# Kernel optimization log

Hardware: AMD Instinct MI355X
Metric: run time of the kernel (lower is better)

The kernel has to match this reference:

```python
import jax, jax.numpy as jnp
import numpy as np

B, S, H, R, IN, OPS, NPAD = 128, 128, 512, 16, 2, 5, 16
L = IN + NPAD
NEG = -1e12


def setup_inputs():
    key = jax.random.key(0)
    ks = jax.random.split(key, 32)
    def n(k, shape, scale=1.0):
        return jax.random.normal(k, shape, jnp.float32) * scale
    s = 0.05
    return {
        "encoder_outputs": n(ks[0], (S, B, H)),
        "current_emb": n(ks[1], (B, 1, H)),
        "left_childs": n(ks[2], (B, H)),
        "padding_hidden": jnp.zeros((1, H), jnp.float32),
        "num_pades": n(ks[3], (B, NPAD, H)),
        "rule_scores": n(ks[4], (R, H)),
        "embedding_weight": n(ks[5], (1, IN, H)),
        "W_concat_l": n(ks[6], (H, H), s), "b_concat_l": jnp.zeros((H,)),
        "W_concat_lg": n(ks[7], (H, H), s), "b_concat_lg": jnp.zeros((H,)),
        "W_concat_r": n(ks[8], (2 * H, H), s), "b_concat_r": jnp.zeros((H,)),
        "W_concat_rg": n(ks[9], (2 * H, H), s), "b_concat_rg": jnp.zeros((H,)),
        "W_tree_attn": n(ks[10], (2 * H, H), s), "b_tree_attn": jnp.zeros((H,)),
        "W_tree_score": n(ks[11], (H, 1), s), "b_tree_score": jnp.zeros((1,)),
        "W_rule_attn": n(ks[12], (2 * H, H), s), "b_rule_attn": jnp.zeros((H,)),
        "W_rule_score": n(ks[13], (H, 1), s), "b_rule_score": jnp.zeros((1,)),
        "W_rp1": n(ks[14], (H, H), s), "b_rp1": jnp.zeros((H,)),
        "W_rp2": n(ks[15], (H, 1), s), "b_rp2": jnp.zeros((1,)),
        "W_sc_attn": n(ks[16], (3 * H, H), s), "b_sc_attn": jnp.zeros((H,)),
        "W_sc_score": n(ks[17], (H, 1), s),
        "W_ops": n(ks[18], (2 * H, OPS), s), "b_ops": jnp.zeros((OPS,)),
        "seq_mask": jax.random.randint(ks[19], (B, S), 0, 2).astype(jnp.int32),
        "mask_nums": jax.random.randint(ks[20], (B, L), 0, 2).astype(jnp.int32),
        "has_left": jax.random.randint(ks[21], (B,), 0, 2).astype(jnp.int32),
        "stack_empty": jax.random.randint(ks[22], (B,), 0, 2).astype(jnp.int32),
    }


def reference(encoder_outputs, current_emb, left_childs, padding_hidden, num_pades,
              rule_scores, embedding_weight,
              W_concat_l, b_concat_l, W_concat_lg, b_concat_lg,
              W_concat_r, b_concat_r, W_concat_rg, b_concat_rg,
              W_tree_attn, b_tree_attn, W_tree_score, b_tree_score,
              W_rule_attn, b_rule_attn, W_rule_score, b_rule_score,
              W_rp1, b_rp1, W_rp2, b_rp2,
              W_sc_attn, b_sc_attn, W_sc_score, W_ops, b_ops,
              seq_mask, mask_nums, has_left, stack_empty):
    sm = seq_mask.astype(bool)          # [B,S] True = pad
    nm = mask_nums.astype(bool)         # [B,L]
    hl = has_left.astype(bool)[:, None]
    se = stack_empty.astype(bool)[:, None]
    h = encoder_outputs.shape[-1]
    # gather top-of-stack embedding, padding for empty stacks (the ragged python loop)
    c = jnp.where(se, padding_hidden[0], current_emb[:, 0])  # [B,H]
    # gated combine: left_child==None branch vs cat(left, c) branch (dropout=eval)
    node_l = jnp.tanh(c @ W_concat_l + b_concat_l) * jax.nn.sigmoid(c @ W_concat_lg + b_concat_lg)
    node_r = (jnp.tanh(left_childs @ W_concat_r[:h] + c @ W_concat_r[h:] + b_concat_r)
              * jax.nn.sigmoid(left_childs @ W_concat_rg[:h] + c @ W_concat_rg[h:] + b_concat_rg))
    q = jnp.where(hl, node_r, node_l)                        # [B,H]
    current_node = q[:, None, :]                              # [B,1,H]
    # TreeAttn: concat(hidden, enc) -> Linear -> tanh -> Linear(H,1) -> softmax over S
    e = jnp.tanh(q @ W_tree_attn[:h] + encoder_outputs @ W_tree_attn[h:] + b_tree_attn)  # [S,B,H]
    ae = (e @ W_tree_score)[..., 0] + b_tree_score[0]         # [S,B]
    ae = jnp.where(sm, NEG, ae.T)                             # [B,S]
    current_attn = jax.nn.softmax(ae, axis=1)                 # [B,S]
    current_context = jnp.einsum('bs,sbh->bh', current_attn, encoder_outputs)[:, None, :]
    # RuleAttn: concat(enc, rule) additive attention, softmax over S
    re = jnp.tanh(encoder_outputs @ W_rule_attn[:h]
                  + (rule_scores @ W_rule_attn[h:])[:, None, None, :]
                  + b_rule_attn)                              # [R,S,B,H]
    r_ae = (re @ W_rule_score)[..., 0] + b_rule_score[0]      # [R,S,B]
    r_ae = jnp.transpose(r_ae, (2, 0, 1))                     # [B,R,S]
    r_ae = jnp.where(sm[:, None, :], NEG, r_ae)
    rules_attn = jax.nn.softmax(r_ae, axis=-1)
    rules_context = jnp.einsum('brs,sbh->brh', rules_attn + 0.2 * current_attn[:, None, :], encoder_outputs)
    rule_prob = jax.nn.softmax((jnp.tanh(rules_context @ W_rp1 + b_rp1) @ W_rp2)[..., 0] + b_rp2[0], axis=-1)  # [B,R]
    # leaf scoring: Score(cat(node, context), [const_embs | num_pades])
    bsz = q.shape[0]
    ew = jnp.concatenate([jnp.broadcast_to(embedding_weight, (bsz,) + embedding_weight.shape[1:]), num_pades], axis=1)  # [B,L,H]
    leaf = jnp.concatenate([q, current_context[:, 0]], axis=1)  # [B,2H]
    sc = jnp.tanh((leaf @ W_sc_attn[:2 * h])[:, None, :] + ew @ W_sc_attn[2 * h:] + b_sc_attn)  # [B,L,H]
    num_score = jnp.where(nm, NEG, (sc @ W_sc_score)[..., 0])   # [B,L]
    op = leaf @ W_ops + b_ops                                   # [B,OPS]
    return num_score, op, current_node, current_context, ew, rule_prob
```

## Files before the change

kernel.cpp:

```cpp
#include <hip/hip_runtime.h>
#include <hip/hip_bf16.h>

#define B_ 128
#define S_ 128
#define H_ 512
#define R_ 16
#define IN_ 2
#define OPS_ 5
#define NPAD_ 16
#define L_ 18
#define NEGV (-1000000000000.0f)
#define C2_ (-2.885390081777927f)

typedef __bf16 bf16_t;
typedef bf16_t bf16x8 __attribute__((ext_vector_type(8)));
typedef float floatx4 __attribute__((ext_vector_type(4)));

__device__ __forceinline__ float rcp_f(float x) { return __builtin_amdgcn_rcpf(x); }
__device__ __forceinline__ float exp2_f(float x) { return __builtin_amdgcn_exp2f(x); }

__device__ __forceinline__ float fast_tanh(float x) {
    return 2.0f * rcp_f(1.0f + exp2_f(C2_ * x)) - 1.0f;
}
__device__ __forceinline__ float fast_sigmoid(float x) {
    return rcp_f(1.0f + exp2_f(-1.4426950408889634f * x));
}
__device__ __forceinline__ unsigned short f2bf(float f) {
    unsigned int u = __builtin_bit_cast(unsigned int, f);
    u += 0x7fff + ((u >> 16) & 1);
    return (unsigned short)(u >> 16);
}
__device__ __forceinline__ float bf2f(unsigned short u) {
    return __builtin_bit_cast(float, (unsigned int)u << 16);
}

__device__ __forceinline__ void glds16(const void* g, void* l) {
    __builtin_amdgcn_global_load_lds(
        (const __attribute__((address_space(1))) void*)g,
        (__attribute__((address_space(3))) void*)l, 16, 0, 0);
}

#define LROW 32
#define LBUF 4096

__device__ __forceinline__ void mfma_tile(const unsigned short* __restrict__ A,
                                          const unsigned short* __restrict__ Bt,
                                          void* __restrict__ Cv, bool bf16_out,
                                          int m0, int n0, int K, int ldc,
                                          unsigned short* As, unsigned short* Bs) {
    const int tid  = threadIdx.x;
    const int w    = tid >> 6, lane = tid & 63;
    const int quad = lane >> 4, mn = lane & 15;
    const int wm = (w & 1) * 64, wn = (w >> 1) * 64;
    const int sr = tid >> 2;
    const int csw = ((tid & 3) ^ ((tid >> 3) & 3)) * 8;
    const int qs  = (quad ^ ((mn >> 1) & 3)) * 8;

    const unsigned short* pa0 = A  + (size_t)(m0 + sr)      * K + csw;
    const unsigned short* pa1 = A  + (size_t)(m0 + sr + 64) * K + csw;
    const unsigned short* pb0 = Bt + (size_t)(n0 + sr)      * K + csw;
    const unsigned short* pb1 = Bt + (size_t)(n0 + sr + 64) * K + csw;

    const int wbase = w * 512;
    glds16(pa0, As + wbase);
    glds16(pa1, As + wbase + 2048);
    glds16(pb0, Bs + wbase);
    glds16(pb1, Bs + wbase + 2048);
    __syncthreads();

    floatx4 acc[4][4] = {};

    for (int k0 = 0; k0 < K; k0 += 32) {
        const int cur = (k0 >> 5) & 1;
        const unsigned short* Asb = As + cur * LBUF;
        const unsigned short* Bsb = Bs + cur * LBUF;

        if (k0 + 32 < K) {
            const int nb = cur ^ 1;
            glds16(pa0 + k0 + 32, As + nb * LBUF + wbase);
            glds16(pa1 + k0 + 32, As + nb * LBUF + wbase + 2048);
            glds16(pb0 + k0 + 32, Bs + nb * LBUF + wbase);
            glds16(pb1 + k0 + 32, Bs + nb * LBUF + wbase + 2048);
        }

        bf16x8 af[4], bfr[4];
        #pragma unroll
        for (int i = 0; i < 4; ++i)
            af[i] = *(const bf16x8*)&Asb[(wm + i * 16 + mn) * LROW + qs];
        #pragma unroll
        for (int j = 0; j < 4; ++j)
            bfr[j] = *(const bf16x8*)&Bsb[(wn + j * 16 + mn) * LROW + qs];

        #pragma unroll
        for (int i = 0; i < 4; ++i)
            #pragma unroll
            for (int j = 0; j < 4; ++j)
                acc[i][j] = __builtin_amdgcn_mfma_f32_16x16x32_bf16(bfr[j], af[i], acc[i][j], 0, 0, 0);

        __syncthreads();
    }

    #pragma unroll
    for (int i = 0; i < 4; ++i) {
        int row = m0 + wm + i * 16 + mn;
        #pragma unroll
        for (int j = 0; j < 4; ++j) {
            int col = n0 + wn + j * 16 + quad * 4;
            if (bf16_out) {
                ushort4 v = {f2bf(acc[i][j][0]), f2bf(acc[i][j][1]),
                             f2bf(acc[i][j][2]), f2bf(acc[i][j][3])};
                *(ushort4*)((unsigned short*)Cv + (size_t)row * ldc + col) = v;
            } else {
                float4 v = {acc[i][j][0], acc[i][j][1], acc[i][j][2], acc[i][j][3]};
                *(float4*)((float*)Cv + (size_t)row * ldc + col) = v;
            }
        }
    }
}

__global__ __launch_bounds__(256) void k_gemm_mega1(const unsigned short* __restrict__ EO_bf,
                                                    const unsigned short* __restrict__ Wcat,
                                                    unsigned short* __restrict__ eobuf,
                                                    const unsigned short* __restrict__ q_bf,
                                                    const unsigned short* __restrict__ T5,
                                                    float* __restrict__ qT) {
    __shared__ unsigned short As[2 * LBUF];
    __shared__ unsigned short Bs[2 * LBUF];
    int blk = blockIdx.x;
    if (blk < 1024)
        mfma_tile(EO_bf, Wcat, eobuf, true, (blk & 127) * 128, (blk >> 7) * 128, 512, 1024, As, Bs);
    else
        mfma_tile(q_bf, T5, qT, false, 0, (blk - 1024) * 128, 512, 512, As, Bs);
}

__global__ __launch_bounds__(256) void k_gemm_mega2(const unsigned short* __restrict__ rctx_bf,
                                                    const unsigned short* __restrict__ T8,
                                                    float* __restrict__ rclin,
                                                    const unsigned short* __restrict__ leaf_bf,
                                                    const unsigned short* __restrict__ T9,
                                                    float* __restrict__ lsb,
                                                    const unsigned short* __restrict__ ew_bf,
                                                    const unsigned short* __restrict__ T10,
                                                    unsigned short* __restrict__ ewp_bf) {
    __shared__ unsigned short As[2 * LBUF];
    __shared__ unsigned short Bs[2 * LBUF];
    int blk = blockIdx.x;
    if (blk < 64)
        mfma_tile(rctx_bf, T8, rclin, false, (blk >> 2) * 128, (blk & 3) * 128, 512, 512, As, Bs);
    else if (blk < 68)
        mfma_tile(leaf_bf, T9, lsb, false, 0, (blk - 64) * 128, 1024, 512, As, Bs);
    else {
        int r = blk - 68;
        mfma_tile(ew_bf, T10, ewp_bf, true, (r >> 2) * 128, (r & 3) * 128, 512, 512, As, Bs);
    }
}

struct MJ5 {
    const unsigned short* A[5]; const unsigned short* Bt[5]; float* C[5];
    int M[5]; int K[5];
};
__global__ __launch_bounds__(256) void gemm_bf16_j5(MJ5 g) {
    __shared__ unsigned short As[2 * LBUF];
    __shared__ unsigned short Bs[2 * LBUF];

    const int z = blockIdx.z;
    const unsigned short* A  = g.A[z];
    const unsigned short* Bt = g.Bt[z];
    float* C = g.C[z];
    const int M = g.M[z], K = g.K[z];

    const int tid  = threadIdx.x;
    const int w    = tid >> 6, lane = tid & 63;
    const int quad = lane >> 4, mn = lane & 15;
    const int wm = (w & 1) * 64, wn = (w >> 1) * 64;
    const int n0 = blockIdx.x * 128;

    const int sr = tid >> 2;
    const int csw = ((tid & 3) ^ ((tid >> 3) & 3)) * 8;
    const int qs  = (quad ^ ((mn >> 1) & 3)) * 8;
    const int ra0 = min(sr, M - 1);
    const int ra1 = min(sr + 64, M - 1);

    const unsigned short* pa0 = A  + (size_t)ra0 * K + csw;
    const unsigned short* pa1 = A  + (size_t)ra1 * K + csw;
    const unsigned short* pb0 = Bt + (size_t)(n0 + sr)      * K + csw;
    const unsigned short* pb1 = Bt + (size_t)(n0 + sr + 64) * K + csw;

    const int wbase = w * 512;
    glds16(pa0, As + wbase);
    glds16(pa1, As + wbase + 2048);
    glds16(pb0, Bs + wbase);
    glds16(pb1, Bs + wbase + 2048);
    __syncthreads();

    floatx4 acc[4][4] = {};

    for (int k0 = 0; k0 < K; k0 += 32) {
        const int cur = (k0 >> 5) & 1;
        const unsigned short* Asb = As + cur * LBUF;
        const unsigned short* Bsb = Bs + cur * LBUF;

        if (k0 + 32 < K) {
            const int nb = cur ^ 1;
            glds16(pa0 + k0 + 32, As + nb * LBUF + wbase);
            glds16(pa1 + k0 + 32, As + nb * LBUF + wbase + 2048);
            glds16(pb0 + k0 + 32, Bs + nb * LBUF + wbase);
            glds16(pb1 + k0 + 32, Bs + nb * LBUF + wbase + 2048);
        }

        bf16x8 af[4], bfr[4];
        #pragma unroll
        for (int i = 0; i < 4; ++i)
            af[i] = *(const bf16x8*)&Asb[(wm + i * 16 + mn) * LROW + qs];
        #pragma unroll
        for (int j = 0; j < 4; ++j)
            bfr[j] = *(const bf16x8*)&Bsb[(wn + j * 16 + mn) * LROW + qs];

        #pragma unroll
        for (int i = 0; i < 4; ++i)
            #pragma unroll
            for (int j = 0; j < 4; ++j)
                acc[i][j] = __builtin_amdgcn_mfma_f32_16x16x32_bf16(bfr[j], af[i], acc[i][j], 0, 0, 0);

        __syncthreads();
    }

    #pragma unroll
    for (int i = 0; i < 4; ++i) {
        int row = wm + i * 16 + mn;
        if (row < M) {
            #pragma unroll
            for (int j = 0; j < 4; ++j) {
                int col = n0 + wn + j * 16 + quad * 4;
                float4 v = {acc[i][j][0], acc[i][j][1], acc[i][j][2], acc[i][j][3]};
                *(float4*)(C + (size_t)row * 512 + col) = v;
            }
        }
    }
}

struct PrepArgs {
    const float *EO, *cur, *padh, *left, *rsc, *embw, *npad;
    const int* se;
    unsigned short *EO_bf, *c_bf, *acat_bf, *rsc_bf, *ew_bf;
    float* ew_out;
    const float* tsrc[11];
    unsigned short* tdst[11];
    int tK[11];
    int tbase[12];
};
#define PG_CAST 8192
#define PG_EW   1152
#define PG_PREP 288
#define PG_WT   3584
#define PG_TOTAL (PG_CAST + PG_EW + PG_PREP + PG_WT)

__global__ __launch_bounds__(256) void k_prep_mega(PrepArgs a) {
    __shared__ float t[32][33];
    int blk = blockIdx.x, tid = threadIdx.x;
    if (blk < PG_CAST) {
        int i = (blk * 256 + tid) * 4;
        float4 v = *(const float4*)(a.EO + i);
        ushort4 o;
        o.x = f2bf(v.x); o.y = f2bf(v.y); o.z = f2bf(v.z); o.w = f2bf(v.w);
        *(ushort4*)(a.EO_bf + i) = o;
    } else if (blk < PG_CAST + PG_EW) {
        int i = ((blk - PG_CAST) * 256 + tid) * 4;
        int j = i & 511;
        int bl = i >> 9;
        int l = bl % L_;
        int b = bl / L_;
        const float* src = (l < IN_) ? (a.embw + l * H_ + j)
                                     : (a.npad + ((size_t)b * NPAD_ + (l - IN_)) * H_ + j);
        float4 v = *(const float4*)src;
        *(float4*)(a.ew_out + i) = v;
        ushort4 o;
        o.x = f2bf(v.x); o.y = f2bf(v.y); o.z = f2bf(v.z); o.w = f2bf(v.w);
        *(ushort4*)(a.ew_bf + i) = o;
    } else if (blk < PG_CAST + PG_EW + PG_PREP) {
        int i = (blk - PG_CAST - PG_EW) * 256 + tid;
        if (i < B_ * H_) {
            int b = i >> 9, j = i & 511;
            float cv = a.se[b] ? a.padh[j] : a.cur[i];
            a.c_bf[i] = f2bf(cv);
            a.acat_bf[b * 1024 + j] = f2bf(a.left[i]);
            a.acat_bf[b * 1024 + 512 + j] = f2bf(cv);
        } else {
            int k = i - B_ * H_;
            a.rsc_bf[k] = f2bf(a.rsc[k]);
        }
    } else {
        int rel = blk - (PG_CAST + PG_EW + PG_PREP);
        int j = 0;
        while (rel >= a.tbase[j + 1]) ++j;
        int r = rel - a.tbase[j];
        int K = a.tK[j];
        const float* src = a.tsrc[j];
        unsigned short* dst = a.tdst[j];
        int bx = (r & 15) * 32;
        int by = (r >> 4) * 32;
        int tx = tid & 31, ty = tid >> 5;
        #pragma unroll
        for (int i = 0; i < 32; i += 8)
            t[ty + i][tx] = src[(size_t)(by + ty + i) * 512 + bx + tx];
        __syncthreads();
        #pragma unroll
        for (int i = 0; i < 32; i += 8)
            dst[(size_t)(bx + ty + i) * K + by + tx] = f2bf(t[tx][ty + i]);
    }
}

__global__ void k_node(const float* __restrict__ gl, const float* __restrict__ glg,
                       const float* __restrict__ gr, const float* __restrict__ grg,
                       const float* __restrict__ bl, const float* __restrict__ blg,
                       const float* __restrict__ br, const float* __restrict__ brg,
                       const int* __restrict__ hl,
                       unsigned short* __restrict__ q_bf, float* __restrict__ node_out,
                       unsigned short* __restrict__ leaf_bf) {
    int i = blockIdx.x * blockDim.x + threadIdx.x;
    int b = i >> 9, j = i & 511;
    float nl = fast_tanh(gl[i] + bl[j]) * fast_sigmoid(glg[i] + blg[j]);
    float nr = fast_tanh(gr[i] + br[j]) * fast_sigmoid(grg[i] + brg[j]);
    float v = hl[b] ? nr : nl;
    node_out[i] = v;
    q_bf[i] = f2bf(v);
    leaf_bf[b * 1024 + j] = f2bf(v);
}

__global__ __launch_bounds__(256) void k_score_fused(const float* __restrict__ qT,
                                                     const unsigned short* __restrict__ eobuf,
                                                     const float* __restrict__ b_ta,
                                                     const float* __restrict__ w_ts,
                                                     const float* __restrict__ b_ts,
                                                     const float* __restrict__ RP,
                                                     const float* __restrict__ b_ra,
                                                     const float* __restrict__ w_rs,
                                                     const float* __restrict__ b_rs,
                                                     const int* __restrict__ sm,
                                                     float* __restrict__ attn,
                                                     float* __restrict__ comb) {
    __shared__ float sc[S_];
    int blk = blockIdx.x;
    int tid = threadIdx.x;
    int wid = tid >> 6, lane = tid & 63;
    int j0 = lane * 8;

    if (blk < 128) {
        int b = blk;
        float4 q0 = *(const float4*)(qT + b * H_ + j0);
        float4 q1 = *(const float4*)(qT + b * H_ + j0 + 4);
        float4 t0 = *(const float4*)(b_ta + j0);
        float4 t1 = *(const float4*)(b_ta + j0 + 4);
        float4 w0 = *(const float4*)(w_ts + j0);
        float4 w1 = *(const float4*)(w_ts + j0 + 4);
        float qc[8] = {C2_*(q0.x+t0.x), C2_*(q0.y+t0.y), C2_*(q0.z+t0.z), C2_*(q0.w+t0.w),
                       C2_*(q1.x+t1.x), C2_*(q1.y+t1.y), C2_*(q1.z+t1.z), C2_*(q1.w+t1.w)};
        float w2[8] = {2*w0.x, 2*w0.y, 2*w0.z, 2*w0.w, 2*w1.x, 2*w1.y, 2*w1.z, 2*w1.w};
        float wsum = 0.5f * (w2[0]+w2[1]+w2[2]+w2[3]+w2[4]+w2[5]+w2[6]+w2[7]);
        float bias = b_ts[0];

        for (int s = wid; s < S_; s += 4) {
            if (sm[b * S_ + s]) {
                if (lane == 0) sc[s] = NEGV;
                continue;
            }
            uint4 ev = *(const uint4*)(eobuf + ((size_t)s * B_ + b) * 1024 + j0);
            const unsigned short* ep = (const unsigned short*)&ev;
            float acc = -wsum;
            #pragma unroll
            for (int k = 0; k < 8; ++k) {
                float y = fmaf(C2_, bf2f(ep[k]), qc[k]);
                acc = fmaf(w2[k], rcp_f(1.0f + exp2_f(y)), acc);
            }
            #pragma unroll
            for (int o = 32; o > 0; o >>= 1) acc += __shfl_xor(acc, o);
            if (lane == 0) sc[s] = acc + bias;
        }
        __syncthreads();
        if (tid < 64) {
            float v0 = sc[tid], v1 = sc[tid + 64];
            float m = fmaxf(v0, v1);
            #pragma unroll
            for (int o = 32; o > 0; o >>= 1) m = fmaxf(m, __shfl_xor(m, o));
            float e0 = __expf(v0 - m), e1 = __expf(v1 - m);
            float ss = e0 + e1;
            #pragma unroll
            for (int o = 32; o > 0; o >>= 1) ss += __shfl_xor(ss, o);
            float r = rcp_f(ss);
            attn[b * S_ + tid] = e0 * r;
            attn[b * S_ + tid + 64] = e1 * r;
        }
        return;
    }

    int row = (blk - 128) * 4 + wid;
    int s = row >> 7, b = row & 127;
    bool masked = sm[b * S_ + s] != 0;
    if (masked) {
        if (lane < R_) comb[((size_t)b * R_ + lane) * S_ + s] = NEGV;
        return;
    }
    uint4 ev = *(const uint4*)(eobuf + (size_t)row * 1024 + 512 + j0);
    const unsigned short* ep = (const unsigned short*)&ev;
    float4 a0 = *(const float4*)(b_ra + j0);
    float4 a1 = *(const float4*)(b_ra + j0 + 4);
    float4 w0 = *(const float4*)(w_rs + j0);
    float4 w1 = *(const float4*)(w_rs + j0 + 4);
    float ba[8] = {a0.x, a0.y, a0.z, a0.w, a1.x, a1.y, a1.z, a1.w};
    float w2[8], ed[8];
    float wsum = 0.f;
    {
        float w[8] = {w0.x, w0.y, w0.z, w0.w, w1.x, w1.y, w1.z, w1.w};
        #pragma unroll
        for (int k = 0; k < 8; ++k) {
            wsum += w[k];
            w2[k] = 2.0f * w[k];
            ed[k] = C2_ * (bf2f(ep[k]) + ba[k]);
        }
    }
    float bias = b_rs[0];
    #pragma unroll
    for (int r = 0; r < R_; ++r) {
        float4 r0 = *(const float4*)(RP + r * H_ + j0);
        float4 r1 = *(const float4*)(RP + r * H_ + j0 + 4);
        float rp[8] = {r0.x, r0.y, r0.z, r0.w, r1.x, r1.y, r1.z, r1.w};
        float acc = -wsum;
        #pragma unroll
        for (int k = 0; k < 8; ++k) {
            float y = fmaf(C2_, rp[k], ed[k]);
            acc = fmaf(w2[k], rcp_f(1.0f + exp2_f(y)), acc);
        }
        #pragma unroll
        for (int o = 32; o > 0; o >>= 1) acc += __shfl_xor(acc, o);
        if (lane == 0) comb[((size_t)b * R_ + r) * S_ + s] = acc + bias;
    }
}

__global__ __launch_bounds__(256) void k_ctxsm(const unsigned short* __restrict__ EO_bf,
                                               const float* __restrict__ attn,
                                               const float* __restrict__ comb,
                                               const int* __restrict__ sm,
                                               float* __restrict__ ctx_out,
                                               unsigned short* __restrict__ leaf_bf,
                                               unsigned short* __restrict__ rctx) {
    __shared__ float cb2[S_ * 20];
    __shared__ float at[S_];
    __shared__ short usl[S_];
    __shared__ int ucount;
    int b = blockIdx.x;
    int tid = threadIdx.x;
    int w = tid >> 6, lane = tid & 63;

    if (tid < S_) at[tid] = attn[b * S_ + tid];
    if (tid == 0) {
        int c = 0;
        for (int s = 0; s < S_; ++s)
            if (!sm[b * S_ + s]) usl[c++] = (short)s;
        ucount = c;
    }
    __syncthreads();

    #pragma unroll
    for (int rr = 0; rr < 4; ++rr) {
        int r = w * 4 + rr;
        const float* rowp = comb + (size_t)b * R_ * S_ + r * S_;
        float v0 = rowp[lane], v1 = rowp[lane + 64];
        float m = fmaxf(v0, v1);
        #pragma unroll
        for (int o = 32; o > 0; o >>= 1) m = fmaxf(m, __shfl_xor(m, o));
        float e0 = __expf(v0 - m), e1 = __expf(v1 - m);
        float ss = e0 + e1;
        #pragma unroll
        for (int o = 32; o > 0; o >>= 1) ss += __shfl_xor(ss, o);
        float rc_ = rcp_f(ss);
        cb2[lane * 20 + r]        = e0 * rc_ + 0.2f * at[lane];
        cb2[(lane + 64) * 20 + r] = e1 * rc_ + 0.2f * at[lane + 64];
    }
    __syncthreads();

    int j = blockIdx.y * 256 + tid;
    int nu = ucount;
    float ctx = 0.f;
    float rc[R_] = {};
    for (int ii = 0; ii < nu; ++ii) {
        int s = usl[ii];
        float eo = bf2f(EO_bf[((size_t)s * B_ + b) * H_ + j]);
        float4 c0 = *(const float4*)&cb2[s * 20];
        float4 c1 = *(const float4*)&cb2[s * 20 + 4];
        float4 c2 = *(const float4*)&cb2[s * 20 + 8];
        float4 c3 = *(const float4*)&cb2[s * 20 + 12];
        ctx = fmaf(at[s], eo, ctx);
        rc[0]  = fmaf(c0.x, eo, rc[0]);  rc[1]  = fmaf(c0.y, eo, rc[1]);
        rc[2]  = fmaf(c0.z, eo, rc[2]);  rc[3]  = fmaf(c0.w, eo, rc[3]);
        rc[4]  = fmaf(c1.x, eo, rc[4]);  rc[5]  = fmaf(c1.y, eo, rc[5]);
        rc[6]  = fmaf(c1.z, eo, rc[6]);  rc[7]  = fmaf(c1.w, eo, rc[7]);
        rc[8]  = fmaf(c2.x, eo, rc[8]);  rc[9]  = fmaf(c2.y, eo, rc[9]);
        rc[10] = fmaf(c2.z, eo, rc[10]); rc[11] = fmaf(c2.w, eo, rc[11]);
        rc[12] = fmaf(c3.x, eo, rc[12]); rc[13] = fmaf(c3.y, eo, rc[13]);
        rc[14] = fmaf(c3.z, eo, rc[14]); rc[15] = fmaf(c3.w, eo, rc[15]);
    }
    ctx_out[b * H_ + j] = ctx;
    leaf_bf[b * 1024 + 512 + j] = f2bf(ctx);
    #pragma unroll
    for (int r = 0; r < R_; ++r) rctx[((size_t)b * R_ + r) * H_ + j] = f2bf(rc[r]);
}

__global__ __launch_bounds__(256) void k_epilogue(const float* __restrict__ rclin,
                                                  const float* __restrict__ b_rp1,
                                                  const float* __restrict__ w_rp2,
                                                  const float* __restrict__ b_rp2,
                                                  float* __restrict__ prob,
                                                  const float* __restrict__ lsb,
                                                  const unsigned short* __restrict__ ewp,
                                                  const float* __restrict__ b_sc,
                                                  const float* __restrict__ w_scs,
                                                  const int* __restrict__ mask_nums,
                                                  float* __restrict__ ns_out,
                                                  const unsigned short* __restrict__ leaf_bf,
                                                  const float* __restrict__ Wops,
                                                  const float* __restrict__ bops,
                                                  float* __restrict__ op_out) {
    __shared__ float sc[R_];
    int blk = blockIdx.x;
    int wid = threadIdx.x >> 6, lane = threadIdx.x & 63;
    if (blk < 128) {
        int b = blk;
        int j0 = lane * 8;
        float4 p0 = *(const float4*)(b_rp1 + j0);
        float4 p1 = *(const float4*)(b_rp1 + j0 + 4);
        float4 w0 = *(const float4*)(w_rp2 + j0);
        float4 w1 = *(const float4*)(w_rp2 + j0 + 4);
        float brc[8] = {C2_*p0.x, C2_*p0.y, C2_*p0.z, C2_*p0.w,
                        C2_*p1.x, C2_*p1.y, C2_*p1.z, C2_*p1.w};
        float w[8] = {w0.x, w0.y, w0.z, w0.w, w1.x, w1.y, w1.z, w1.w};
        float wsum = 0.f;
        #pragma unroll
        for (int k = 0; k < 8; ++k) wsum += w[k];
        #pragma unroll
        for (int rr = 0; rr < 4; ++rr) {
            int r = wid * 4 + rr;
            const float* rl = rclin + ((size_t)b * R_ + r) * H_ + j0;
            float4 r0 = *(const float4*)(rl);
            float4 r1 = *(const float4*)(rl + 4);
            float rv[8] = {r0.x, r0.y, r0.z, r0.w, r1.x, r1.y, r1.z, r1.w};
            float acc = -wsum;
            #pragma unroll
            for (int k = 0; k < 8; ++k) {
                float y = fmaf(C2_, rv[k], brc[k]);
                acc = fmaf(2.0f * w[k], rcp_f(1.0f + exp2_f(y)), acc);
            }
            #pragma unroll
            for (int o = 32; o > 0; o >>= 1) acc += __shfl_xor(acc, o);
            if (lane == 0) sc[r] = acc + b_rp2[0];
        }
        __syncthreads();
        if (threadIdx.x < R_) {
            float m = -1e30f;
            for (int r = 0; r < R_; ++r) m = fmaxf(m, sc[r]);
            float sum = 0.f;
            for (int r = 0; r < R_; ++r) sum += __expf(sc[r] - m);
            prob[b * R_ + threadIdx.x] = __expf(sc[threadIdx.x] - m) * rcp_f(sum);
        }
    } else if (blk < 704) {
        int row = (blk - 128) * 4 + wid;
        int b = row / L_, l = row - b * L_;
        bool masked = mask_nums[b * L_ + l] != 0;
        if (masked) {
            if (lane == 0) ns_out[b * L_ + l] = NEGV;
            return;
        }
        int j0 = lane * 8;
        uint4 ev = *(const uint4*)(ewp + (size_t)row * H_ + j0);
        const unsigned short* ep = (const unsigned short*)&ev;
        float4 l0 = *(const float4*)(lsb + b * H_ + j0);
        float4 l1 = *(const float4*)(lsb + b * H_ + j0 + 4);
        float4 s0 = *(const float4*)(b_sc + j0);
        float4 s1 = *(const float4*)(b_sc + j0 + 4);
        float4 w0 = *(const float4*)(w_scs + j0);
        float4 w1 = *(const float4*)(w_scs + j0 + 4);
        float lc[8] = {C2_*(l0.x+s0.x), C2_*(l0.y+s0.y), C2_*(l0.z+s0.z), C2_*(l0.w+s0.w),
                       C2_*(l1.x+s1.x), C2_*(l1.y+s1.y), C2_*(l1.z+s1.z), C2_*(l1.w+s1.w)};
        float w[8] = {w0.x, w0.y, w0.z, w0.w, w1.x, w1.y, w1.z, w1.w};
        float wsum = 0.f;
        #pragma unroll
        for (int k = 0; k < 8; ++k) wsum += w[k];
        float acc = -wsum;
        #pragma unroll
        for (int k = 0; k < 8; ++k) {
            float y = fmaf(C2_, bf2f(ep[k]), lc[k]);
            acc = fmaf(2.0f * w[k], rcp_f(1.0f + exp2_f(y)), acc);
        }
        #pragma unroll
        for (int o = 32; o > 0; o >>= 1) acc += __shfl_xor(acc, o);
        if (lane == 0) ns_out[b * L_ + l] = acc;
    } else {
        int b = (blk - 704) * 4 + wid;
        int base = b * 1024 + lane * 16;
        uint4 v0 = *(const uint4*)(leaf_bf + base);
        uint4 v1 = *(const uint4*)(leaf_bf + base + 8);
        const unsigned short* lp0 = (const unsigned short*)&v0;
        const unsigned short* lp1 = (const unsigned short*)&v1;
        float lv[16];
        #pragma unroll
        for (int k = 0; k < 8; ++k) { lv[k] = bf2f(lp0[k]); lv[8 + k] = bf2f(lp1[k]); }
        #pragma unroll
        for (int o = 0; o < OPS_; ++o) {
            float acc = 0.f;
            #pragma unroll
            for (int k = 0; k < 16; ++k)
                acc = fmaf(lv[k], Wops[(size_t)(lane * 16 + k) * OPS_ + o], acc);
            #pragma unroll
            for (int of = 32; of > 0; of >>= 1) acc += __shfl_xor(acc, of);
            if (lane == 0) op_out[b * OPS_ + o] = acc + bops[o];
        }
    }
}

extern "C" void kernel_launch(void* const* d_in, const int* in_sizes, int n_in,
                              void* d_out, int out_size, void* d_ws, size_t ws_size,
                              hipStream_t stream) {
    const float* EO   = (const float*)d_in[0];
    const float* cur  = (const float*)d_in[1];
    const float* left = (const float*)d_in[2];
    const float* padh = (const float*)d_in[3];
    const float* npad = (const float*)d_in[4];
    const float* rsc  = (const float*)d_in[5];
    const float* embw = (const float*)d_in[6];
    const float* Wl   = (const float*)d_in[7];  const float* bl   = (const float*)d_in[8];
    const float* Wlg  = (const float*)d_in[9];  const float* blg  = (const float*)d_in[10];
    const float* Wr   = (const float*)d_in[11]; const float* br   = (const float*)d_in[12];
    const float* Wrg  = (const float*)d_in[13]; const float* brg  = (const float*)d_in[14];
    const float* Wta  = (const float*)d_in[15]; const float* bta  = (const float*)d_in[16];
    const float* Wts  = (const float*)d_in[17]; const float* bts  = (const float*)d_in[18];
    const float* Wra  = (const float*)d_in[19]; const float* bra  = (const float*)d_in[20];
    const float* Wrs  = (const float*)d_in[21]; const float* brs  = (const float*)d_in[22];
    const float* Wrp1 = (const float*)d_in[23]; const float* brp1 = (const float*)d_in[24];
    const float* Wrp2 = (const float*)d_in[25]; const float* brp2 = (const float*)d_in[26];
    const float* Wsa  = (const float*)d_in[27]; const float* bsa  = (const float*)d_in[28];
    const float* Wss  = (const float*)d_in[29];
    const float* Wops = (const float*)d_in[30]; const float* bops = (const float*)d_in[31];
    const int* smk = (const int*)d_in[32];
    const int* nmk = (const int*)d_in[33];
    const int* hlk = (const int*)d_in[34];
    const int* sek = (const int*)d_in[35];

    float* out = (float*)d_out;

    const size_t O_NS    = 0;
    const size_t O_OP    = O_NS + (size_t)B_ * L_;
    const size_t O_NODE  = O_OP + (size_t)B_ * OPS_;
    const size_t O_CTX   = O_NODE + (size_t)B_ * H_;
    const size_t O_EW    = O_CTX + (size_t)B_ * H_;
    const size_t O_RPROB = O_EW + (size_t)B_ * L_ * H_;

    float* f = (float*)d_ws;
    float* rp_buf = f;               f += 8192;
    float* qT     = f;               f += 65536;
    float* attn   = f;               f += 16384;
    float* comb   = f;               f += 262144;
    float* gl     = f;               f += 65536;
    float* glg    = f;               f += 65536;
    float* gr     = f;               f += 65536;
    float* grg    = f;               f += 65536;
    float* lsb    = f;               f += 65536;
    float* rclin  = f;               f += 1048576;
    unsigned short* u = (unsigned short*)f;
    unsigned short* EO_bf   = u;     u += 8388608;
    unsigned short* ew_bf   = u;     u += 1179648;
    unsigned short* leaf_bf = u;     u += 131072;
    unsigned short* rctx_bf = u;     u += 1048576;
    unsigned short* Wcat    = u;     u += 524288;
    unsigned short* T0      = u;     u += 262144;
    unsigned short* T1      = u;     u += 262144;
    unsigned short* T2      = u;     u += 524288;
    unsigned short* T3      = u;     u += 524288;
    unsigned short* T4      = u;     u += 262144;
    unsigned short* T5      = u;     u += 262144;
    unsigned short* T8      = u;     u += 262144;
    unsigned short* T9      = u;     u += 524288;
    unsigned short* T10     = u;     u += 262144;
    unsigned short* q_bf    = u;     u += 65536;
    unsigned short* c_bf    = u;     u += 65536;
    unsigned short* acat_bf = u;     u += 131072;
    unsigned short* rsc_bf  = u;     u += 8192;
    unsigned short* ewp_bf  = u;     u += 1179648;
    unsigned short* eobuf   = u;     u += 16777216;

    PrepArgs a;
    a.EO = EO; a.cur = cur; a.padh = padh; a.left = left; a.rsc = rsc;
    a.embw = embw; a.npad = npad; a.se = sek;
    a.EO_bf = EO_bf; a.c_bf = c_bf; a.acat_bf = acat_bf; a.rsc_bf = rsc_bf;
    a.ew_bf = ew_bf; a.ew_out = out + O_EW;
    const float* tsrc[11] = {Wl, Wlg, Wr, Wrg, Wra + (size_t)H_ * H_, Wta,
                             Wta + (size_t)H_ * H_, Wra, Wrp1, Wsa, Wsa + (size_t)2 * H_ * H_};
    unsigned short* tdst[11] = {T0, T1, T2, T3, T4, T5, Wcat, Wcat + 512 * 512, T8, T9, T10};
    int tk[11] = {512, 512, 1024, 1024, 512, 512, 512, 512, 512, 1024, 512};
    int base = 0;
    for (int i = 0; i < 11; ++i) {
        a.tsrc[i] = tsrc[i]; a.tdst[i] = tdst[i]; a.tK[i] = tk[i];
        a.tbase[i] = base;
        base += 16 * (tk[i] / 32);
    }
    a.tbase[11] = base;
    k_prep_mega<<<PG_TOTAL, 256, 0, stream>>>(a);

    MJ5 g;
    g.A[0] = c_bf;    g.Bt[0] = T0; g.C[0] = gl;     g.M[0] = B_;  g.K[0] = 512;
    g.A[1] = c_bf;    g.Bt[1] = T1; g.C[1] = glg;    g.M[1] = B_;  g.K[1] = 512;
    g.A[2] = acat_bf; g.Bt[2] = T2; g.C[2] = gr;     g.M[2] = B_;  g.K[2] = 1024;
    g.A[3] = acat_bf; g.Bt[3] = T3; g.C[3] = grg;    g.M[3] = B_;  g.K[3] = 1024;
    g.A[4] = rsc_bf;  g.Bt[4] = T4; g.C[4] = rp_buf; g.M[4] = R_;  g.K[4] = 512;
    gemm_bf16_j5<<<dim3(4, 1, 5), 256, 0, stream>>>(g);

    k_node<<<256, 256, 0, stream>>>(gl, glg, gr, grg, bl, blg, br, brg, hlk,
                                    q_bf, out + O_NODE, leaf_bf);

    k_gemm_mega1<<<1028, 256, 0, stream>>>(EO_bf, Wcat, eobuf, q_bf, T5, qT);

    k_score_fused<<<128 + S_ * B_ / 4, 256, 0, stream>>>(
        qT, eobuf, bta, Wts, bts, rp_buf, bra, Wrs, brs, smk, attn, comb);

    k_ctxsm<<<dim3(B_, 2), 256, 0, stream>>>(EO_bf, attn, comb, smk, out + O_CTX,
                                             leaf_bf, rctx_bf);

    k_gemm_mega2<<<140, 256, 0, stream>>>(rctx_bf, T8, rclin, leaf_bf, T9, lsb,
                                          ew_bf, T10, ewp_bf);

    k_epilogue<<<736, 256, 0, stream>>>(rclin, brp1, Wrp2, brp2, out + O_RPROB,
                                        lsb, ewp_bf, bsa, Wss, nmk, out + O_NS,
                                        leaf_bf, Wops, bops, out + O_OP);
}
```

Measured before the change: 290.0 us.

## Fuse EO bf16 cast and node gating into GEMM A-operand staging

Replaces the global_load_lds GEMM tile with a register-staged version. It can convert fp32 encoder outputs to bf16 on the fly, or compute the tanh·sigmoid node gating while loading A. The separate EO cast pass (8192 blocks) and the k_node kernel go away, which removes a full bf16 copy of the encoder outputs and one launch. B fragments are now read straight from global memory into registers instead of through LDS. k_ctxsm reads fp32 EO directly. The trade-off is double the A-read bandwidth in the big GEMM, and B loads that no longer pass through LDS.

```diff
diff --git a/kernel.cpp b/kernel.cpp
--- a/kernel.cpp
+++ b/kernel.cpp
@@ -33,104 +33,176 @@
 __device__ __forceinline__ float bf2f(unsigned short u) {
     return __builtin_bit_cast(float, (unsigned int)u << 16);
 }
-
-__device__ __forceinline__ void glds16(const void* g, void* l) {
-    __builtin_amdgcn_global_load_lds(
-        (const __attribute__((address_space(1))) void*)g,
-        (__attribute__((address_space(3))) void*)l, 16, 0, 0);
-}
-
-#define LROW 32
-#define LBUF 4096
-
-__device__ __forceinline__ void mfma_tile(const unsigned short* __restrict__ A,
-                                          const unsigned short* __restrict__ Bt,
-                                          void* __restrict__ Cv, bool bf16_out,
-                                          int m0, int n0, int K, int ldc,
-                                          unsigned short* As, unsigned short* Bs) {
+__device__ __forceinline__ unsigned int pk2(unsigned short a, unsigned short b) {
+    return (unsigned int)a | ((unsigned int)b << 16);
+}
+
+#define LSTRA 40
+#define LBUFA 5120
+
+struct GateArgs {
+    const float *gl, *glg, *gr, *grg, *bl, *blg, *br, *brg;
+    const int* hl;
+    float* node_out;
+    unsigned short* leaf_bf;
+};
+
+template <int AMODE>
+__device__ __forceinline__ uint4 stage_load(const void* A, const GateArgs& ga,
+                                            int row, int kc, int K) {
+    if constexpr (AMODE == 0) {
+        return *(const uint4*)((const unsigned short*)A + (size_t)row * K + kc);
+    } else if constexpr (AMODE == 1) {
+        const float* Af = (const float*)A;
+        float4 v0 = *(const float4*)(Af + (size_t)row * K + kc);
+        float4 v1 = *(const float4*)(Af + (size_t)row * K + kc + 4);
+        uint4 r;
+        r.x = pk2(f2bf(v0.x), f2bf(v0.y));
+        r.y = pk2(f2bf(v0.z), f2bf(v0.w));
+        r.z = pk2(f2bf(v1.x), f2bf(v1.y));
+        r.w = pk2(f2bf(v1.z), f2bf(v1.w));
+        return r;
+    } else {
+        int hlr = ga.hl[row];
+        const float* ts = (hlr ? ga.gr  : ga.gl ) + (size_t)row * 512 + kc;
+        const float* ss = (hlr ? ga.grg : ga.glg) + (size_t)row * 512 + kc;
+        const float* tb = (hlr ? ga.br  : ga.bl ) + kc;
+        const float* sb = (hlr ? ga.brg : ga.blg) + kc;
+        float4 t0 = *(const float4*)ts, t1 = *(const float4*)(ts + 4);
+        float4 s0 = *(const float4*)ss, s1 = *(const float4*)(ss + 4);
+        float4 u0 = *(const float4*)tb, u1 = *(const float4*)(tb + 4);
+        float4 w0 = *(const float4*)sb, w1 = *(const float4*)(sb + 4);
+        float v[8];
+        v[0] = fast_tanh(t0.x + u0.x) * fast_sigmoid(s0.x + w0.x);
+        v[1] = fast_tanh(t0.y + u0.y) * fast_sigmoid(s0.y + w0.y);
+        v[2] = fast_tanh(t0.z + u0.z) * fast_sigmoid(s0.z + w0.z);
+        v[3] = fast_tanh(t0.w + u0.w) * fast_sigmoid(s0.w + w0.w);
+        v[4] = fast_tanh(t1.x + u1.x) * fast_sigmoid(s1.x + w1.x);
+        v[5] = fast_tanh(t1.y + u1.y) * fast_sigmoid(s1.y + w1.y);
+        v[6] = fast_tanh(t1.z + u1.z) * fast_sigmoid(s1.z + w1.z);
+        v[7] = fast_tanh(t1.w + u1.w) * fast_sigmoid(s1.w + w1.w);
+        uint4 r;
+        r.x = pk2(f2bf(v[0]), f2bf(v[1]));
+        r.y = pk2(f2bf(v[2]), f2bf(v[3]));
+        r.z = pk2(f2bf(v[4]), f2bf(v[5]));
+        r.w = pk2(f2bf(v[6]), f2bf(v[7]));
+        if (ga.node_out) {
+            float4 o0 = {v[0], v[1], v[2], v[3]};
+            float4 o1 = {v[4], v[5], v[6], v[7]};
+            *(float4*)(ga.node_out + (size_t)row * 512 + kc) = o0;
+            *(float4*)(ga.node_out + (size_t)row * 512 + kc + 4) = o1;
+            *(uint4*)(ga.leaf_bf + (size_t)row * 1024 + kc) = r;
+        }
+        return r;
+    }
+}
+
+template <int AMODE>
+__device__ __forceinline__ void mfma_tileX(const void* A, const GateArgs& ga,
+                                           const unsigned short* Bt, void* Cv,
+                                           bool bf16_out, int m0, int n0, int K,
+                                           int ldc, int M, unsigned short* As) {
     const int tid  = threadIdx.x;
     const int w    = tid >> 6, lane = tid & 63;
     const int quad = lane >> 4, mn = lane & 15;
     const int wm = (w & 1) * 64, wn = (w >> 1) * 64;
     const int sr = tid >> 2;
-    const int csw = ((tid & 3) ^ ((tid >> 3) & 3)) * 8;
-    const int qs  = (quad ^ ((mn >> 1) & 3)) * 8;
-
-    const unsigned short* pa0 = A  + (size_t)(m0 + sr)      * K + csw;
-    const unsigned short* pa1 = A  + (size_t)(m0 + sr + 64) * K + csw;
-    const unsigned short* pb0 = Bt + (size_t)(n0 + sr)      * K + csw;
-    const unsigned short* pb1 = Bt + (size_t)(n0 + sr + 64) * K + csw;
-
-    const int wbase = w * 512;
-    glds16(pa0, As + wbase);
-    glds16(pa1, As + wbase + 2048);
-    glds16(pb0, Bs + wbase);
-    glds16(pb1, Bs + wbase + 2048);
+    const int sc = (tid & 3) * 8;
+    const int ar0 = m0 + min(sr, M - 1);
+    const int ar1 = m0 + min(sr + 64, M - 1);
+
+    const unsigned short* pB = Bt + (size_t)(n0 + wn + mn) * K + quad * 8;
+
+    uint4 a0 = stage_load<AMODE>(A, ga, ar0, sc, K);
+    uint4 a1 = stage_load<AMODE>(A, ga, ar1, sc, K);
+    *(uint4*)&As[sr * LSTRA + sc]        = a0;
+    *(uint4*)&As[(sr + 64) * LSTRA + sc] = a1;
+    uint4 a0n = a0, a1n = a1;
+    if (K > 32) {
+        a0n = stage_load<AMODE>(A, ga, ar0, 32 + sc, K);
+        a1n = stage_load<AMODE>(A, ga, ar1, 32 + sc, K);
+    }
+    bf16x8 bcur[4];
+    #pragma unroll
+    for (int j = 0; j < 4; ++j)
+        bcur[j] = *(const bf16x8*)(pB + (size_t)j * 16 * K);
     __syncthreads();
 
     floatx4 acc[4][4] = {};
 
     for (int k0 = 0; k0 < K; k0 += 32) {
         const int cur = (k0 >> 5) & 1;
-        const unsigned short* Asb = As + cur * LBUF;
-        const unsigned short* Bsb = Bs + cur * LBUF;
-
+        bf16x8 bnext[4];
         if (k0 + 32 < K) {
-            const int nb = cur ^ 1;
-            glds16(pa0 + k0 + 32, As + nb * LBUF + wbase);
-            glds16(pa1 + k0 + 32, As + nb * LBUF + wbase + 2048);
-            glds16(pb0 + k0 + 32, Bs + nb * LBUF + wbase);
-            glds16(pb1 + k0 + 32, Bs + nb * LBUF + wbase + 2048);
-        }
-
-        bf16x8 af[4], bfr[4];
+            #pragma unroll
+            for (int j = 0; j < 4; ++j)
+                bnext[j] = *(const bf16x8*)(pB + (size_t)j * 16 * K + k0 + 32);
+        }
+        const unsigned short* Asb = As + cur * LBUFA;
+        bf16x8 af[4];
         #pragma unroll
         for (int i = 0; i < 4; ++i)
-            af[i] = *(const bf16x8*)&Asb[(wm + i * 16 + mn) * LROW + qs];
-        #pragma unroll
-        for (int j = 0; j < 4; ++j)
-            bfr[j] = *(const bf16x8*)&Bsb[(wn + j * 16 + mn) * LROW + qs];
+            af[i] = *(const bf16x8*)&Asb[(wm + i * 16 + mn) * LSTRA + quad * 8];
 
         #pragma unroll
         for (int i = 0; i < 4; ++i)
             #pragma unroll
             for (int j = 0; j < 4; ++j)
-                acc[i][j] = __builtin_amdgcn_mfma_f32_16x16x32_bf16(bfr[j], af[i], acc[i][j], 0, 0, 0);
-
-        __syncthreads();
+                acc[i][j] = __builtin_amdgcn_mfma_f32_16x16x32_bf16(bcur[j], af[i], acc[i][j], 0, 0, 0);
+
+        if (k0 + 32 < K) {
+            unsigned short* Asn = As + (cur ^ 1) * LBUFA;
+            *(uint4*)&Asn[sr * LSTRA + sc]        = a0n;
+            *(uint4*)&Asn[(sr + 64) * LSTRA + sc] = a1n;
+            if (k0 + 64 < K) {
+                a0n = stage_load<AMODE>(A, ga, ar0, k0 + 64 + sc, K);
+                a1n = stage_load<AMODE>(A, ga, ar1, k0 + 64 + sc, K);
+            }
+            __syncthreads();
+            #pragma unroll
+            for (int j = 0; j < 4; ++j) bcur[j] = bnext[j];
+        }
     }
 
     #pragma unroll
     for (int i = 0; i < 4; ++i) {
-        int row = m0 + wm + i * 16 + mn;
-        #pragma unroll
-        for (int j = 0; j < 4; ++j) {
-            int col = n0 + wn + j * 16 + quad * 4;
-            if (bf16_out) {
-                ushort4 v = {f2bf(acc[i][j][0]), f2bf(acc[i][j][1]),
-                             f2bf(acc[i][j][2]), f2bf(acc[i][j][3])};
-                *(ushort4*)((unsigned short*)Cv + (size_t)row * ldc + col) = v;
-            } else {
-                float4 v = {acc[i][j][0], acc[i][j][1], acc[i][j][2], acc[i][j][3]};
-                *(float4*)((float*)Cv + (size_t)row * ldc + col) = v;
+        int lrow = wm + i * 16 + mn;
+        if (lrow < M) {
+            int row = m0 + lrow;
+            #pragma unroll
+            for (int j = 0; j < 4; ++j) {
+                int col = n0 + wn + j * 16 + quad * 4;
+                if (bf16_out) {
+                    ushort4 v = {f2bf(acc[i][j][0]), f2bf(acc[i][j][1]),
+                                 f2bf(acc[i][j][2]), f2bf(acc[i][j][3])};
+                    *(ushort4*)((unsigned short*)Cv + (size_t)row * ldc + col) = v;
+                } else {
+                    float4 v = {acc[i][j][0], acc[i][j][1], acc[i][j][2], acc[i][j][3]};
+                    *(float4*)((float*)Cv + (size_t)row * ldc + col) = v;
+                }
             }
         }
     }
 }
 
-__global__ __launch_bounds__(256) void k_gemm_mega1(const unsigned short* __restrict__ EO_bf,
+__global__ __launch_bounds__(256) void k_gemm_mega1(const float* __restrict__ EO,
                                                     const unsigned short* __restrict__ Wcat,
                                                     unsigned short* __restrict__ eobuf,
-                                                    const unsigned short* __restrict__ q_bf,
+                                                    GateArgs ga,
                                                     const unsigned short* __restrict__ T5,
                                                     float* __restrict__ qT) {
-    __shared__ unsigned short As[2 * LBUF];
-    __shared__ unsigned short Bs[2 * LBUF];
+    __shared__ unsigned short As[2 * LBUFA];
     int blk = blockIdx.x;
-    if (blk < 1024)
-        mfma_tile(EO_bf, Wcat, eobuf, true, (blk & 127) * 128, (blk >> 7) * 128, 512, 1024, As, Bs);
-    else
-        mfma_tile(q_bf, T5, qT, false, 0, (blk - 1024) * 128, 512, 512, As, Bs);
+    if (blk < 1024) {
+        GateArgs d{};
+        mfma_tileX<1>(EO, d, Wcat, eobuf, true, (blk & 127) * 128, (blk >> 7) * 128,
+                      512, 1024, 128, As);
+    } else {
+        int nb = blk - 1024;
+        GateArgs g2 = ga;
+        if (nb != 0) { g2.node_out = nullptr; g2.leaf_bf = nullptr; }
+        mfma_tileX<2>(nullptr, g2, T5, qT, false, 0, nb * 128, 512, 512, 128, As);
+    }
 }
 
 __global__ __launch_bounds__(256) void k_gemm_mega2(const unsigned short* __restrict__ rctx_bf,
@@ -142,16 +214,18 @@
                                                     const unsigned short* __restrict__ ew_bf,
                                                     const unsigned short* __restrict__ T10,
                                                     unsigned short* __restrict__ ewp_bf) {
-    __shared__ unsigned short As[2 * LBUF];
-    __shared__ unsigned short Bs[2 * LBUF];
+    __shared__ unsigned short As[2 * LBUFA];
+    GateArgs d{};
     int blk = blockIdx.x;
     if (blk < 64)
-        mfma_tile(rctx_bf, T8, rclin, false, (blk >> 2) * 128, (blk & 3) * 128, 512, 512, As, Bs);
+        mfma_tileX<0>(rctx_bf, d, T8, rclin, false, (blk >> 2) * 128, (blk & 3) * 128,
+                      512, 512, 128, As);
     else if (blk < 68)
-        mfma_tile(leaf_bf, T9, lsb, false, 0, (blk - 64) * 128, 1024, 512, As, Bs);
+        mfma_tileX<0>(leaf_bf, d, T9, lsb, false, 0, (blk - 64) * 128, 1024, 512, 128, As);
     else {
         int r = blk - 68;
-        mfma_tile(ew_bf, T10, ewp_bf, true, (r >> 2) * 128, (r & 3) * 128, 512, 512, As, Bs);
+        mfma_tileX<0>(ew_bf, d, T10, ewp_bf, true, (r >> 2) * 128, (r & 3) * 128,
+                      512, 512, 128, As);
     }
 }
 
@@ -160,112 +234,33 @@
     int M[5]; int K[5];
 };
 __global__ __launch_bounds__(256) void gemm_bf16_j5(MJ5 g) {
-    __shared__ unsigned short As[2 * LBUF];
-    __shared__ unsigned short Bs[2 * LBUF];
-
-    const int z = blockIdx.z;
-    const unsigned short* A  = g.A[z];
-    const unsigned short* Bt = g.Bt[z];
-    float* C = g.C[z];
-    const int M = g.M[z], K = g.K[z];
-
-    const int tid  = threadIdx.x;
-    const int w    = tid >> 6, lane = tid & 63;
-    const int quad = lane >> 4, mn = lane & 15;
-    const int wm = (w & 1) * 64, wn = (w >> 1) * 64;
-    const int n0 = blockIdx.x * 128;
-
-    const int sr = tid >> 2;
-    const int csw = ((tid & 3) ^ ((tid >> 3) & 3)) * 8;
-    const int qs  = (quad ^ ((mn >> 1) & 3)) * 8;
-    const int ra0 = min(sr, M - 1);
-    const int ra1 = min(sr + 64, M - 1);
-
-    const unsigned short* pa0 = A  + (size_t)ra0 * K + csw;
-    const unsigned short* pa1 = A  + (size_t)ra1 * K + csw;
-    const unsigned short* pb0 = Bt + (size_t)(n0 + sr)      * K + csw;
-    const unsigned short* pb1 = Bt + (size_t)(n0 + sr + 64) * K + csw;
-
-    const int wbase = w * 512;
-    glds16(pa0, As + wbase);
-    glds16(pa1, As + wbase + 2048);
-    glds16(pb0, Bs + wbase);
-    glds16(pb1, Bs + wbase + 2048);
-    __syncthreads();
-
-    floatx4 acc[4][4] = {};
-
-    for (int k0 = 0; k0 < K; k0 += 32) {
-        const int cur = (k0 >> 5) & 1;
-        const unsigned short* Asb = As + cur * LBUF;
-        const unsigned short* Bsb = Bs + cur * LBUF;
-
-        if (k0 + 32 < K) {
-            const int nb = cur ^ 1;
-            glds16(pa0 + k0 + 32, As + nb * LBUF + wbase);
-            glds16(pa1 + k0 + 32, As + nb * LBUF + wbase + 2048);
-            glds16(pb0 + k0 + 32, Bs + nb * LBUF + wbase);
-            glds16(pb1 + k0 + 32, Bs + nb * LBUF + wbase + 2048);
-        }
-
-        bf16x8 af[4], bfr[4];
-        #pragma unroll
-        for (int i = 0; i < 4; ++i)
-            af[i] = *(const bf16x8*)&Asb[(wm + i * 16 + mn) * LROW + qs];
-        #pragma unroll
-        for (int j = 0; j < 4; ++j)
-            bfr[j] = *(const bf16x8*)&Bsb[(wn + j * 16 + mn) * LROW + qs];
-
-        #pragma unroll
-        for (int i = 0; i < 4; ++i)
-            #pragma unroll
-            for (int j = 0; j < 4; ++j)
-                acc[i][j] = __builtin_amdgcn_mfma_f32_16x16x32_bf16(bfr[j], af[i], acc[i][j], 0, 0, 0);
-
-        __syncthreads();
-    }
-
-    #pragma unroll
-    for (int i = 0; i < 4; ++i) {
-        int row = wm + i * 16 + mn;
-        if (row < M) {
-            #pragma unroll
-            for (int j = 0; j < 4; ++j) {
-                int col = n0 + wn + j * 16 + quad * 4;
-                float4 v = {acc[i][j][0], acc[i][j][1], acc[i][j][2], acc[i][j][3]};
-                *(float4*)(C + (size_t)row * 512 + col) = v;
-            }
-        }
-    }
+    __shared__ unsigned short As[2 * LBUFA];
+    GateArgs d{};
+    int z = blockIdx.z;
+    mfma_tileX<0>(g.A[z], d, g.Bt[z], g.C[z], false, 0, blockIdx.x * 128,
+                  g.K[z], 512, g.M[z], As);
 }
 
 struct PrepArgs {
-    const float *EO, *cur, *padh, *left, *rsc, *embw, *npad;
+    const float *cur, *padh, *left, *rsc, *embw, *npad;
     const int* se;
-    unsigned short *EO_bf, *c_bf, *acat_bf, *rsc_bf, *ew_bf;
+    unsigned short *c_bf, *acat_bf, *rsc_bf, *ew_bf;
     float* ew_out;
     const float* tsrc[11];
     unsigned short* tdst[11];
     int tK[11];
     int tbase[12];
 };
-#define PG_CAST 8192
 #define PG_EW   1152
 #define PG_PREP 288
 #define PG_WT   3584
-#define PG_TOTAL (PG_CAST + PG_EW + PG_PREP + PG_WT)
+#define PG_TOTAL (PG_EW + PG_PREP + PG_WT)
 
 __global__ __launch_bounds__(256) void k_prep_mega(PrepArgs a) {
     __shared__ float t[32][33];
     int blk = blockIdx.x, tid = threadIdx.x;
-    if (blk < PG_CAST) {
+    if (blk < PG_EW) {
         int i = (blk * 256 + tid) * 4;
-        float4 v = *(const float4*)(a.EO + i);
-        ushort4 o;
-        o.x = f2bf(v.x); o.y = f2bf(v.y); o.z = f2bf(v.z); o.w = f2bf(v.w);
-        *(ushort4*)(a.EO_bf + i) = o;
-    } else if (blk < PG_CAST + PG_EW) {
-        int i = ((blk - PG_CAST) * 256 + tid) * 4;
         int j = i & 511;
         int bl = i >> 9;
         int l = bl % L_;
@@ -277,8 +272,8 @@
         ushort4 o;
         o.x = f2bf(v.x); o.y = f2bf(v.y); o.z = f2bf(v.z); o.w = f2bf(v.w);
         *(ushort4*)(a.ew_bf + i) = o;
-    } else if (blk < PG_CAST + PG_EW + PG_PREP) {
-        int i = (blk - PG_CAST - PG_EW) * 256 + tid;
+    } else if (blk < PG_EW + PG_PREP) {
+        int i = (blk - PG_EW) * 256 + tid;
         if (i < B_ * H_) {
             int b = i >> 9, j = i & 511;
             float cv = a.se[b] ? a.padh[j] : a.cur[i];
@@ -290,7 +285,7 @@
             a.rsc_bf[k] = f2bf(a.rsc[k]);
         }
     } else {
-        int rel = blk - (PG_CAST + PG_EW + PG_PREP);
+        int rel = blk - (PG_EW + PG_PREP);
         int j = 0;
         while (rel >= a.tbase[j + 1]) ++j;
         int r = rel - a.tbase[j];
@@ -308,23 +303,6 @@
         for (int i = 0; i < 32; i += 8)
             dst[(size_t)(bx + ty + i) * K + by + tx] = f2bf(t[tx][ty + i]);
     }
-}
-
-__global__ void k_node(const float* __restrict__ gl, const float* __restrict__ glg,
-                       const float* __restrict__ gr, const float* __restrict__ grg,
-                       const float* __restrict__ bl, const float* __restrict__ blg,
-                       const float* __restrict__ br, const float* __restrict__ brg,
-                       const int* __restrict__ hl,
-                       unsigned short* __restrict__ q_bf, float* __restrict__ node_out,
-                       unsigned short* __restrict__ leaf_bf) {
-    int i = blockIdx.x * blockDim.x + threadIdx.x;
-    int b = i >> 9, j = i & 511;
-    float nl = fast_tanh(gl[i] + bl[j]) * fast_sigmoid(glg[i] + blg[j]);
-    float nr = fast_tanh(gr[i] + br[j]) * fast_sigmoid(grg[i] + brg[j]);
-    float v = hl[b] ? nr : nl;
-    node_out[i] = v;
-    q_bf[i] = f2bf(v);
-    leaf_bf[b * 1024 + j] = f2bf(v);
 }
 
 __global__ __launch_bounds__(256) void k_score_fused(const float* __restrict__ qT,
@@ -436,7 +414,7 @@
     }
 }
 
-__global__ __launch_bounds__(256) void k_ctxsm(const unsigned short* __restrict__ EO_bf,
+__global__ __launch_bounds__(256) void k_ctxsm(const float* __restrict__ EO,
                                                const float* __restrict__ attn,
                                                const float* __restrict__ comb,
                                                const int* __restrict__ sm,
@@ -484,7 +462,7 @@
     float rc[R_] = {};
     for (int ii = 0; ii < nu; ++ii) {
         int s = usl[ii];
-        float eo = bf2f(EO_bf[((size_t)s * B_ + b) * H_ + j]);
+        float eo = EO[((size_t)s * B_ + b) * H_ + j];
         float4 c0 = *(const float4*)&cb2[s * 20];
         float4 c1 = *(const float4*)&cb2[s * 20 + 4];
         float4 c2 = *(const float4*)&cb2[s * 20 + 8];
@@ -665,7 +643,6 @@
     float* lsb    = f;               f += 65536;
     float* rclin  = f;               f += 1048576;
     unsigned short* u = (unsigned short*)f;
-    unsigned short* EO_bf   = u;     u += 8388608;
     unsigned short* ew_bf   = u;     u += 1179648;
     unsigned short* leaf_bf = u;     u += 131072;
     unsigned short* rctx_bf = u;     u += 1048576;
@@ -679,7 +656,6 @@
     unsigned short* T8      = u;     u += 262144;
     unsigned short* T9      = u;     u += 524288;
     unsigned short* T10     = u;     u += 262144;
-    unsigned short* q_bf    = u;     u += 65536;
     unsigned short* c_bf    = u;     u += 65536;
     unsigned short* acat_bf = u;     u += 131072;
     unsigned short* rsc_bf  = u;     u += 8192;
@@ -687,9 +663,9 @@
     unsigned short* eobuf   = u;     u += 16777216;
 
     PrepArgs a;
-    a.EO = EO; a.cur = cur; a.padh = padh; a.left = left; a.rsc = rsc;
+    a.cur = cur; a.padh = padh; a.left = left; a.rsc = rsc;
     a.embw = embw; a.npad = npad; a.se = sek;
-    a.EO_bf = EO_bf; a.c_bf = c_bf; a.acat_bf = acat_bf; a.rsc_bf = rsc_bf;
+    a.c_bf = c_bf; a.acat_bf = acat_bf; a.rsc_bf = rsc_bf;
     a.ew_bf = ew_bf; a.ew_out = out + O_EW;
     const float* tsrc[11] = {Wl, Wlg, Wr, Wrg, Wra + (size_t)H_ * H_, Wta,
                              Wta + (size_t)H_ * H_, Wra, Wrp1, Wsa, Wsa + (size_t)2 * H_ * H_};
@@ -712,15 +688,16 @@
     g.A[4] = rsc_bf;  g.Bt[4] = T4; g.C[4] = rp_buf; g.M[4] = R_;  g.K[4] = 512;
     gemm_bf16_j5<<<dim3(4, 1, 5), 256, 0, stream>>>(g);
 
-    k_node<<<256, 256, 0, stream>>>(gl, glg, gr, grg, bl, blg, br, brg, hlk,
-                                    q_bf, out + O_NODE, leaf_bf);
-
-    k_gemm_mega1<<<1028, 256, 0, stream>>>(EO_bf, Wcat, eobuf, q_bf, T5, qT);
+    GateArgs ga;
+    ga.gl = gl; ga.glg = glg; ga.gr = gr; ga.grg = grg;
+    ga.bl = bl; ga.blg = blg; ga.br = br; ga.brg = brg;
+    ga.hl = hlk; ga.node_out = out + O_NODE; ga.leaf_bf = leaf_bf;
+    k_gemm_mega1<<<1028, 256, 0, stream>>>(EO, Wcat, eobuf, ga, T5, qT);
 
     k_score_fused<<<128 + S_ * B_ / 4, 256, 0, stream>>>(
         qT, eobuf, bta, Wts, bts, rp_buf, bra, Wrs, brs, smk, attn, comb);
 
-    k_ctxsm<<<dim3(B_, 2), 256, 0, stream>>>(EO_bf, attn, comb, smk, out + O_CTX,
+    k_ctxsm<<<dim3(B_, 2), 256, 0, stream>>>(EO, attn, comb, smk, out + O_CTX,
                                              leaf_bf, rctx_bf);
 
     k_gemm_mega2<<<140, 256, 0, stream>>>(rctx_bf, T8, rclin, leaf_bf, T9, lsb,
```

New measurement: 364.4 us. 25.7% more time.
